# Optimization experiments

Measured on AMD Instinct MI355X. Metric: run time of the kernel, lower is better.

Reference implementation:

```python
import jax, jax.numpy as jnp
import numpy as np

B, T, C, H, NUM_EDGE_TYPES = 2, 512, 256, 8, 16


def setup_inputs() -> dict:
    key = jax.random.key(0)
    ks = jax.random.split(key, 8)
    init = 0.02
    x = jax.random.normal(ks[0], (B, T, C), dtype=jnp.float32)
    bias_matrix = jax.random.randint(ks[1], (B, T, T), 0, NUM_EDGE_TYPES)
    w_attn = jax.random.normal(ks[2], (C, 3 * C), dtype=jnp.float32) * init
    w_proj = jax.random.normal(ks[3], (C, C), dtype=jnp.float32) * init
    w_edge_k = jax.random.normal(ks[4], (C, C), dtype=jnp.float32) * init
    w_edge_v = jax.random.normal(ks[5], (C, C), dtype=jnp.float32) * init
    edge_emb_table = jax.random.normal(ks[6], (NUM_EDGE_TYPES, C), dtype=jnp.float32)
    attn_bias_table = jax.random.normal(ks[7], (NUM_EDGE_TYPES, H), dtype=jnp.float32)
    return {
        "x": x,
        "bias_matrix": bias_matrix,
        "w_attn": w_attn,
        "w_proj": w_proj,
        "w_edge_k": w_edge_k,
        "w_edge_v": w_edge_v,
        "edge_emb_table": edge_emb_table,
        "attn_bias_table": attn_bias_table,
    }


def reference(x, bias_matrix, w_attn, w_proj, w_edge_k, w_edge_v,
              edge_emb_table, attn_bias_table):
    b, t, c = x.shape
    h = attn_bias_table.shape[1]
    e = c // h
    scale = jnp.sqrt(jnp.asarray(e, x.dtype))

    qkv = x @ w_attn                              # (B,T,3C)
    q, k, v = jnp.split(qkv, 3, axis=-1)
    # (B,H,T,E)
    q = q.reshape(b, t, h, e).transpose(0, 2, 1, 3)
    k = k.reshape(b, t, h, e).transpose(0, 2, 1, 3)
    v = v.reshape(b, t, h, e).transpose(0, 2, 1, 3)

    # edge-type embeddings and per-pair k/v modulation, (B,T,T,H,E)
    ee = edge_emb_table[bias_matrix]              # (B,T,T,C)
    e_k = (ee @ w_edge_k).reshape(b, t, t, h, e)
    e_v = (ee @ w_edge_v).reshape(b, t, t, h, e)

    # scores[b,h,i,j] = sum_e q[b,h,i,e] * k[b,h,j,e] * e_k[b, j, i, h, e]
    # (torch: e_k permuted to (B,H,j,i,E), broadcast-multiplied by k then
    #  contracted with q via 'bhie,bhjie->bhij')
    scores = jnp.einsum('bhie,bhje,bjihe->bhij', q, k, e_k) / scale

    causal = jnp.tril(jnp.ones((t, t), dtype=bool))  # (T,T)
    scores = jnp.where(causal, scores, -jnp.inf)

    # edge-type attention bias: (B,T,T,H) -> (B,H,T,T), zeroed above diagonal
    bias = attn_bias_table[bias_matrix].transpose(0, 3, 1, 2)
    bias = jnp.where(causal, bias, jnp.zeros((), bias.dtype))

    attn = jax.nn.softmax(scores + bias, axis=-1)  # (B,H,T,T)

    # y[b,h,i,e] = sum_j attn[b,h,i,j] * v[b,h,j,e] * e_v[b, j, i, h, e]
    y = jnp.einsum('bhij,bhje,bjihe->bhie', attn, v, e_v)
    y = y.transpose(0, 2, 1, 3).reshape(b, t, c)
    return y @ w_proj
```

## Files before the change

kernel.cpp:

```cpp
#include <hip/hip_runtime.h>
#include <hip/hip_bf16.h>
#include <math.h>

#define Bdim 2
#define Tdim 512
#define Cdim 256
#define Hdim 8
#define Edim 32
#define NTYPES 16
#define TI 8
#define JT 128

__global__ __launch_bounds__(256) void pre_kernel(
    const float* __restrict__ A, const float* __restrict__ Bw,
    const float* __restrict__ emb, const float* __restrict__ wk,
    const float* __restrict__ wv,
    float* __restrict__ qT, float* __restrict__ kT, float* __restrict__ vT,
    float* __restrict__ ekt, float* __restrict__ evt)
{
    __shared__ float smem[16 * 34 + 16 * 64];
    int tid = threadIdx.x;

    if (blockIdx.x >= 384) {
        int t = blockIdx.x - 384;
        float* se = smem;
        se[tid] = emb[t * Cdim + tid];
        __syncthreads();
        float a = 0.f, b = 0.f;
        for (int k = 0; k < Cdim; ++k) {
            float ev = se[k];
            a = fmaf(ev, wk[k * Cdim + tid], a);
            b = fmaf(ev, wv[k * Cdim + tid], b);
        }
        ekt[t * Cdim + tid] = a;
        evt[t * Cdim + tid] = b;
        return;
    }

    const int N = 3 * Cdim;
    const int K = Cdim;
    float (*As)[34] = (float(*)[34])smem;
    float (*Bs)[64] = (float(*)[64])(smem + 16 * 34);
    int m0 = (blockIdx.x / 12) * 32;
    int n0 = (blockIdx.x % 12) * 64;
    int tr = tid >> 4, tc = tid & 15;
    float acc[2][4] = {};
    int bkr = tid >> 4, bcq = (tid & 15) * 4;

    for (int k0 = 0; k0 < K; k0 += 16) {
        if (tid < 128) {
            int r = tid >> 2, kq = (tid & 3) * 4;
            float4 av = *(const float4*)(A + (size_t)(m0 + r) * K + k0 + kq);
            As[kq + 0][r] = av.x;
            As[kq + 1][r] = av.y;
            As[kq + 2][r] = av.z;
            As[kq + 3][r] = av.w;
        }
        float4 bv = *(const float4*)(Bw + (size_t)(k0 + bkr) * N + n0 + bcq);
        *(float4*)&Bs[bkr][bcq] = bv;
        __syncthreads();
#pragma unroll
        for (int kk = 0; kk < 16; ++kk) {
            float2 a2 = *(float2*)&As[kk][tr * 2];
            float4 b4 = *(float4*)&Bs[kk][tc * 4];
            acc[0][0] = fmaf(a2.x, b4.x, acc[0][0]);
            acc[0][1] = fmaf(a2.x, b4.y, acc[0][1]);
            acc[0][2] = fmaf(a2.x, b4.z, acc[0][2]);
            acc[0][3] = fmaf(a2.x, b4.w, acc[0][3]);
            acc[1][0] = fmaf(a2.y, b4.x, acc[1][0]);
            acc[1][1] = fmaf(a2.y, b4.y, acc[1][1]);
            acc[1][2] = fmaf(a2.y, b4.z, acc[1][2]);
            acc[1][3] = fmaf(a2.y, b4.w, acc[1][3]);
        }
        __syncthreads();
    }
    int sec = n0 >> 8;
    float* dst = (sec == 0) ? qT : (sec == 1) ? kT : vT;
    int cc0 = (n0 & 255) + tc * 4;
    int h = cc0 >> 5;
    int e0 = cc0 & 31;
#pragma unroll
    for (int i = 0; i < 2; ++i) {
        int m = m0 + tr * 2 + i;
        int bq = m >> 9, t = m & (Tdim - 1);
        float4 val = make_float4(acc[i][0], acc[i][1], acc[i][2], acc[i][3]);
        *(float4*)&dst[(((size_t)bq * Hdim + h) * Tdim + t) * Edim + e0] = val;
    }
}

__global__ __launch_bounds__(512, 4) void attn_kernel(
    const float* __restrict__ qT, const float* __restrict__ kT,
    const float* __restrict__ vT, const int* __restrict__ bm,
    const float* __restrict__ ekt, const float* __restrict__ evt,
    const float* __restrict__ abt, float* __restrict__ y)
{
    __shared__ float kv[JT][36];
    __shared__ float qm[TI][NTYPES][36];
    __shared__ float ss[TI][516];
    __shared__ unsigned int st1pf[Tdim];
    __shared__ unsigned int st2pf[Tdim];
    __shared__ float sekt[NTYPES][36];
    __shared__ float sevt[NTYPES][36];
    __shared__ float sq[TI][36];
    __shared__ float sabt[NTYPES];
    __shared__ float sinv[TI];

    float* spart = (float*)qm;

    const int pairIdx = blockIdx.x;
    const int bh = blockIdx.y;
    const int h = bh & (Hdim - 1);
    const int b = bh >> 3;
    const int tid = threadIdx.x;
    const int wave = tid >> 6;
    const int lane = tid & 63;
    const float inv_scale = 0.17677669529663687f;

    const float* qbase = qT + (size_t)bh * Tdim * Edim;
    const float* kbase = kT + (size_t)bh * Tdim * Edim;
    const float* vbase = vT + (size_t)bh * Tdim * Edim;
    const int* bmb = bm + (size_t)b * Tdim * Tdim;

    if (tid < 128) {
        int t = tid >> 3, eq = tid & 7;
        *(float4*)&sekt[t][eq * 4] = *(const float4*)&ekt[t * Cdim + h * Edim + eq * 4];
        *(float4*)&sevt[t][eq * 4] = *(const float4*)&evt[t * Cdim + h * Edim + eq * 4];
    }
    if (tid < NTYPES) sabt[tid] = abt[tid * Hdim + h];

    for (int rep = 0; rep < 2; ++rep) {
        int tau = rep ? (63 - pairIdx) : pairIdx;
        int i0 = tau * TI;
        int imax = i0 + TI - 1;
        int njt = (imax >> 7) + 1;
        int jmax = njt << 7;

        __syncthreads();

        if (tid < TI * 8) {
            int r = tid >> 3, eq = tid & 7;
            *(float4*)&sq[r][eq * 4] =
                *(const float4*)&qbase[(size_t)(i0 + r) * Edim + eq * 4];
        }
        if (tid < jmax) {
            const int* rowp = bmb + (size_t)tid * Tdim + i0;
            int4 lo = *(const int4*)rowp;
            int4 hi = *(const int4*)(rowp + 4);
            st1pf[tid] =
                ((unsigned)(lo.x & 15)) | (((unsigned)(lo.y & 15)) << 4) |
                (((unsigned)(lo.z & 15)) << 8) | (((unsigned)(lo.w & 15)) << 12) |
                (((unsigned)(hi.x & 15)) << 16) | (((unsigned)(hi.y & 15)) << 20) |
                (((unsigned)(hi.z & 15)) << 24) | (((unsigned)(hi.w & 15)) << 28);
            unsigned w2 = 0;
#pragma unroll
            for (int iiq = 0; iiq < 8; ++iiq)
                w2 |= ((unsigned)(bmb[(size_t)(i0 + iiq) * Tdim + tid] & 15)) << (iiq * 4);
            st2pf[tid] = w2;
        }
        {
            int r0 = tid >> 3, eq0 = tid & 7;
            *(float4*)&kv[r0][eq0 * 4] =
                *(const float4*)&kbase[(size_t)r0 * Edim + eq0 * 4];
            int idx1 = tid + 512;
            int r1 = idx1 >> 3, eq1 = idx1 & 7;
            *(float4*)&kv[r1][eq1 * 4] =
                *(const float4*)&kbase[(size_t)r1 * Edim + eq1 * 4];
        }
        __syncthreads();
        for (int idx = tid; idx < TI * NTYPES * 8; idx += 512) {
            int eq = idx & 7;
            int t = (idx >> 3) & (NTYPES - 1);
            int r = idx >> 7;
            float4 qv = *(float4*)&sq[r][eq * 4];
            float4 ev = *(float4*)&sekt[t][eq * 4];
            float4 o;
            o.x = qv.x * ev.x; o.y = qv.y * ev.y;
            o.z = qv.z * ev.z; o.w = qv.w * ev.w;
            *(float4*)&qm[r][t][eq * 4] = o;
        }

        for (int jt = 0; jt < njt; ++jt) {
            int j0 = jt << 7;
            if (jt > 0) {
                __syncthreads();
                for (int idx = tid; idx < JT * 8; idx += 512) {
                    int r = idx >> 3, eq = idx & 7;
                    *(float4*)&kv[r][eq * 4] =
                        *(const float4*)&kbase[(size_t)(j0 + r) * Edim + eq * 4];
                }
            }
            __syncthreads();

            int jsub = wave & 1;
            int jl = (jsub << 6) + lane;
            int j = j0 + jl;
            float4 k4[8];
#pragma unroll
            for (int eq = 0; eq < 8; ++eq) k4[eq] = *(float4*)&kv[jl][eq * 4];
            unsigned tp = st1pf[j];
            unsigned tp2 = st2pf[j];

#pragma unroll
            for (int u = 0; u < 2; ++u) {
                int ii = (wave >> 1) + (u << 2);
                int i = i0 + ii;
                if (j0 + (jsub << 6) > i) continue;
                int t1 = (tp >> (ii * 4)) & 15;
                int t2 = (tp2 >> (ii * 4)) & 15;
                float s = 0.f;
#pragma unroll
                for (int eq = 0; eq < 8; ++eq) {
                    float4 qv = *(float4*)&qm[ii][t1][eq * 4];
                    s = fmaf(qv.x, k4[eq].x, s);
                    s = fmaf(qv.y, k4[eq].y, s);
                    s = fmaf(qv.z, k4[eq].z, s);
                    s = fmaf(qv.w, k4[eq].w, s);
                }
                if (j <= i) ss[ii][j] = s * inv_scale + sabt[t2];
            }
        }
        __syncthreads();

        {
            int r0 = tid >> 3, eq0 = tid & 7;
            *(float4*)&kv[r0][eq0 * 4] =
                *(const float4*)&vbase[(size_t)r0 * Edim + eq0 * 4];
            int idx1 = tid + 512;
            int r1 = idx1 >> 3, eq1 = idx1 & 7;
            *(float4*)&kv[r1][eq1 * 4] =
                *(const float4*)&vbase[(size_t)r1 * Edim + eq1 * 4];
        }
        {
            int ii = wave;
            int i = i0 + ii;
            float m = -1e30f;
            for (int j = lane; j <= i; j += 64) m = fmaxf(m, ss[ii][j]);
            for (int off = 32; off; off >>= 1) m = fmaxf(m, __shfl_xor(m, off));
            float sum = 0.f;
            for (int j = lane; j <= i; j += 64) {
                float p = __expf(ss[ii][j] - m);
                ss[ii][j] = p;
                sum += p;
            }
            for (int off = 32; off; off >>= 1) sum += __shfl_xor(sum, off);
            if (lane == 0) sinv[ii] = 1.0f / sum;
        }

        float4 acc[TI];
#pragma unroll
        for (int ii = 0; ii < TI; ++ii) acc[ii] = make_float4(0.f, 0.f, 0.f, 0.f);
        int gid = tid >> 3;
        int eqg = tid & 7;
        for (int jt = 0; jt < njt; ++jt) {
            int j0 = jt << 7;
            if (jt > 0) {
                __syncthreads();
                for (int idx = tid; idx < JT * 8; idx += 512) {
                    int r = idx >> 3, eq = idx & 7;
                    *(float4*)&kv[r][eq * 4] =
                        *(const float4*)&vbase[(size_t)(j0 + r) * Edim + eq * 4];
                }
            }
            __syncthreads();
#pragma unroll
            for (int sub = 0; sub < 2; ++sub) {
                int jl = (sub << 6) + gid;
                int j = j0 + jl;
                float4 v4 = *(float4*)&kv[jl][eqg * 4];
                unsigned tp = st1pf[j];
#pragma unroll
                for (int ii = 0; ii < TI; ++ii) {
                    int i = i0 + ii;
                    if (j0 + (sub << 6) > i) continue;
                    float p = (j <= i) ? ss[ii][j] : 0.f;
                    int t1 = (tp >> (ii * 4)) & 15;
                    float4 ev = *(float4*)&sevt[t1][eqg * 4];
                    acc[ii].x = fmaf(p * ev.x, v4.x, acc[ii].x);
                    acc[ii].y = fmaf(p * ev.y, v4.y, acc[ii].y);
                    acc[ii].z = fmaf(p * ev.z, v4.z, acc[ii].z);
                    acc[ii].w = fmaf(p * ev.w, v4.w, acc[ii].w);
                }
            }
        }
#pragma unroll
        for (int ii = 0; ii < TI; ++ii) {
#pragma unroll
            for (int m = 8; m <= 32; m <<= 1) {
                acc[ii].x += __shfl_xor(acc[ii].x, m);
                acc[ii].y += __shfl_xor(acc[ii].y, m);
                acc[ii].z += __shfl_xor(acc[ii].z, m);
                acc[ii].w += __shfl_xor(acc[ii].w, m);
            }
        }
        if (lane < 8) {
#pragma unroll
            for (int ii = 0; ii < TI; ++ii)
                *(float4*)&spart[((wave * TI + ii) << 5) + lane * 4] = acc[ii];
        }
        __syncthreads();
        if (tid < TI * Edim) {
            int ii = tid >> 5, e = tid & 31;
            float yv = 0.f;
#pragma unroll
            for (int w = 0; w < 8; ++w) yv += spart[((w * TI + ii) << 5) + e];
            yv *= sinv[ii];
            y[((size_t)(b * Tdim + i0 + ii)) * Cdim + h * Edim + e] = yv;
        }
    }
}

__global__ __launch_bounds__(256) void proj_gemm_kernel(
    const float* __restrict__ A, const float* __restrict__ Bw,
    float* __restrict__ out)
{
    const int N = Cdim;
    const int K = Cdim;
    __shared__ float As[16][34];
    __shared__ float Bs[16][64];
    int m0 = blockIdx.y * 32;
    int n0 = blockIdx.x * 64;
    int tid = threadIdx.x;
    int tr = tid >> 4, tc = tid & 15;
    float acc[2][4] = {};
    int bkr = tid >> 4, bcq = (tid & 15) * 4;

    for (int k0 = 0; k0 < K; k0 += 16) {
        if (tid < 128) {
            int r = tid >> 2, kq = (tid & 3) * 4;
            float4 av = *(const float4*)(A + (size_t)(m0 + r) * K + k0 + kq);
            As[kq + 0][r] = av.x;
            As[kq + 1][r] = av.y;
            As[kq + 2][r] = av.z;
            As[kq + 3][r] = av.w;
        }
        float4 bv = *(const float4*)(Bw + (size_t)(k0 + bkr) * N + n0 + bcq);
        *(float4*)&Bs[bkr][bcq] = bv;
        __syncthreads();
#pragma unroll
        for (int kk = 0; kk < 16; ++kk) {
            float2 a2 = *(float2*)&As[kk][tr * 2];
            float4 b4 = *(float4*)&Bs[kk][tc * 4];
            acc[0][0] = fmaf(a2.x, b4.x, acc[0][0]);
            acc[0][1] = fmaf(a2.x, b4.y, acc[0][1]);
            acc[0][2] = fmaf(a2.x, b4.z, acc[0][2]);
            acc[0][3] = fmaf(a2.x, b4.w, acc[0][3]);
            acc[1][0] = fmaf(a2.y, b4.x, acc[1][0]);
            acc[1][1] = fmaf(a2.y, b4.y, acc[1][1]);
            acc[1][2] = fmaf(a2.y, b4.z, acc[1][2]);
            acc[1][3] = fmaf(a2.y, b4.w, acc[1][3]);
        }
        __syncthreads();
    }
#pragma unroll
    for (int i = 0; i < 2; ++i) {
        int m = m0 + tr * 2 + i;
        float4 val = make_float4(acc[i][0], acc[i][1], acc[i][2], acc[i][3]);
        *(float4*)&out[(size_t)m * N + n0 + tc * 4] = val;
    }
}

extern "C" void kernel_launch(void* const* d_in, const int* in_sizes, int n_in,
                              void* d_out, int out_size, void* d_ws, size_t ws_size,
                              hipStream_t stream) {
    (void)in_sizes; (void)n_in; (void)out_size; (void)ws_size;
    const float* x = (const float*)d_in[0];
    const int* bias_matrix = (const int*)d_in[1];
    const float* w_attn = (const float*)d_in[2];
    const float* w_proj = (const float*)d_in[3];
    const float* w_edge_k = (const float*)d_in[4];
    const float* w_edge_v = (const float*)d_in[5];
    const float* edge_emb = (const float*)d_in[6];
    const float* attn_bias = (const float*)d_in[7];
    float* out = (float*)d_out;

    const size_t n_qkv = (size_t)Bdim * Hdim * Tdim * Edim;
    float* ws = (float*)d_ws;
    float* qT = ws;
    float* kT = qT + n_qkv;
    float* vT = kT + n_qkv;
    float* y = vT + n_qkv;
    float* ekt = y + (size_t)Bdim * Tdim * Cdim;
    float* evt = ekt + (size_t)NTYPES * Cdim;

    pre_kernel<<<400, 256, 0, stream>>>(x, w_attn, edge_emb, w_edge_k, w_edge_v,
                                        qT, kT, vT, ekt, evt);
    attn_kernel<<<dim3(32, 16), 512, 0, stream>>>(qT, kT, vT, bias_matrix,
                                                  ekt, evt, attn_bias, y);
    proj_gemm_kernel<<<dim3(4, 32), 256, 0, stream>>>(y, w_proj, out);
}
```

Baseline: 133.5 us.

## Double-buffer K/V tiles with register prefetch and XOR-swizzled shared layout

Converts the single K/V shared-memory tile into a ping-pong pair. The next 128-row tile is loaded into registers before the current tile's score or accumulation work and stored into the other buffer afterwards, so global-load latency overlaps compute and one barrier per tile is dropped. The padded row stride of 36 is replaced by a 32-float stride with an XOR swizzle to avoid bank conflicts. This costs extra shared memory and registers for the prefetch, which at 512 threads with a launch bound of 4 could reduce occupancy.

```diff
diff --git a/kernel.cpp b/kernel.cpp
--- a/kernel.cpp
+++ b/kernel.cpp
@@ -94,7 +94,7 @@
     const float* __restrict__ ekt, const float* __restrict__ evt,
     const float* __restrict__ abt, float* __restrict__ y)
 {
-    __shared__ float kv[JT][36];
+    __shared__ float kv[2][JT][32];
     __shared__ float qm[TI][NTYPES][36];
     __shared__ float ss[TI][516];
     __shared__ unsigned int st1pf[Tdim];
@@ -120,6 +120,10 @@
     const float* kbase = kT + (size_t)bh * Tdim * Edim;
     const float* vbase = vT + (size_t)bh * Tdim * Edim;
     const int* bmb = bm + (size_t)b * Tdim * Tdim;
+
+    const int sr0 = tid >> 3;
+    const int seq4 = (tid & 7) << 2;
+    const int ssw = seq4 ^ ((sr0 & 7) << 2);
 
     if (tid < 128) {
         int t = tid >> 3, eq = tid & 7;
@@ -157,15 +161,10 @@
                 w2 |= ((unsigned)(bmb[(size_t)(i0 + iiq) * Tdim + tid] & 15)) << (iiq * 4);
             st2pf[tid] = w2;
         }
-        {
-            int r0 = tid >> 3, eq0 = tid & 7;
-            *(float4*)&kv[r0][eq0 * 4] =
-                *(const float4*)&kbase[(size_t)r0 * Edim + eq0 * 4];
-            int idx1 = tid + 512;
-            int r1 = idx1 >> 3, eq1 = idx1 & 7;
-            *(float4*)&kv[r1][eq1 * 4] =
-                *(const float4*)&kbase[(size_t)r1 * Edim + eq1 * 4];
-        }
+        *(float4*)&kv[0][sr0][ssw] =
+            *(const float4*)&kbase[((size_t)sr0 << 5) + seq4];
+        *(float4*)&kv[0][sr0 + 64][ssw] =
+            *(const float4*)&kbase[(((size_t)sr0 + 64) << 5) + seq4];
         __syncthreads();
         for (int idx = tid; idx < TI * NTYPES * 8; idx += 512) {
             int eq = idx & 7;
@@ -178,25 +177,27 @@
             o.z = qv.z * ev.z; o.w = qv.w * ev.w;
             *(float4*)&qm[r][t][eq * 4] = o;
         }
-
+        __syncthreads();
+
+        int cur = 0;
         for (int jt = 0; jt < njt; ++jt) {
             int j0 = jt << 7;
-            if (jt > 0) {
-                __syncthreads();
-                for (int idx = tid; idx < JT * 8; idx += 512) {
-                    int r = idx >> 3, eq = idx & 7;
-                    *(float4*)&kv[r][eq * 4] =
-                        *(const float4*)&kbase[(size_t)(j0 + r) * Edim + eq * 4];
-                }
-            }
-            __syncthreads();
+            const bool pf = (jt + 1) < njt;
+            float4 n0, n1;
+            if (pf) {
+                const float* src = kbase + ((size_t)(j0 + 128) << 5);
+                n0 = *(const float4*)(src + ((size_t)sr0 << 5) + seq4);
+                n1 = *(const float4*)(src + (((size_t)sr0 + 64) << 5) + seq4);
+            }
 
             int jsub = wave & 1;
             int jl = (jsub << 6) + lane;
             int j = j0 + jl;
+            const int xsw = (jl & 7) << 2;
             float4 k4[8];
 #pragma unroll
-            for (int eq = 0; eq < 8; ++eq) k4[eq] = *(float4*)&kv[jl][eq * 4];
+            for (int eq = 0; eq < 8; ++eq)
+                k4[eq] = *(float4*)&kv[cur][jl][(eq << 2) ^ xsw];
             unsigned tp = st1pf[j];
             unsigned tp2 = st2pf[j];
 
@@ -218,18 +219,20 @@
                 }
                 if (j <= i) ss[ii][j] = s * inv_scale + sabt[t2];
             }
-        }
-        __syncthreads();
-
-        {
-            int r0 = tid >> 3, eq0 = tid & 7;
-            *(float4*)&kv[r0][eq0 * 4] =
-                *(const float4*)&vbase[(size_t)r0 * Edim + eq0 * 4];
-            int idx1 = tid + 512;
-            int r1 = idx1 >> 3, eq1 = idx1 & 7;
-            *(float4*)&kv[r1][eq1 * 4] =
-                *(const float4*)&vbase[(size_t)r1 * Edim + eq1 * 4];
-        }
+
+            if (pf) {
+                *(float4*)&kv[cur ^ 1][sr0][ssw] = n0;
+                *(float4*)&kv[cur ^ 1][sr0 + 64][ssw] = n1;
+            }
+            __syncthreads();
+            cur ^= 1;
+        }
+
+        *(float4*)&kv[0][sr0][ssw] =
+            *(const float4*)&vbase[((size_t)sr0 << 5) + seq4];
+        *(float4*)&kv[0][sr0 + 64][ssw] =
+            *(const float4*)&vbase[(((size_t)sr0 + 64) << 5) + seq4];
+
         {
             int ii = wave;
             int i = i0 + ii;
@@ -245,28 +248,28 @@
             for (int off = 32; off; off >>= 1) sum += __shfl_xor(sum, off);
             if (lane == 0) sinv[ii] = 1.0f / sum;
         }
+        __syncthreads();
 
         float4 acc[TI];
 #pragma unroll
         for (int ii = 0; ii < TI; ++ii) acc[ii] = make_float4(0.f, 0.f, 0.f, 0.f);
         int gid = tid >> 3;
-        int eqg = tid & 7;
+        int eqg4 = (tid & 7) << 2;
+        cur = 0;
         for (int jt = 0; jt < njt; ++jt) {
             int j0 = jt << 7;
-            if (jt > 0) {
-                __syncthreads();
-                for (int idx = tid; idx < JT * 8; idx += 512) {
-                    int r = idx >> 3, eq = idx & 7;
-                    *(float4*)&kv[r][eq * 4] =
-                        *(const float4*)&vbase[(size_t)(j0 + r) * Edim + eq * 4];
-                }
-            }
-            __syncthreads();
+            const bool pf = (jt + 1) < njt;
+            float4 n0, n1;
+            if (pf) {
+                const float* src = vbase + ((size_t)(j0 + 128) << 5);
+                n0 = *(const float4*)(src + ((size_t)sr0 << 5) + seq4);
+                n1 = *(const float4*)(src + (((size_t)sr0 + 64) << 5) + seq4);
+            }
 #pragma unroll
             for (int sub = 0; sub < 2; ++sub) {
                 int jl = (sub << 6) + gid;
                 int j = j0 + jl;
-                float4 v4 = *(float4*)&kv[jl][eqg * 4];
+                float4 v4 = *(float4*)&kv[cur][jl][eqg4 ^ ((jl & 7) << 2)];
                 unsigned tp = st1pf[j];
 #pragma unroll
                 for (int ii = 0; ii < TI; ++ii) {
@@ -274,13 +277,19 @@
                     if (j0 + (sub << 6) > i) continue;
                     float p = (j <= i) ? ss[ii][j] : 0.f;
                     int t1 = (tp >> (ii * 4)) & 15;
-                    float4 ev = *(float4*)&sevt[t1][eqg * 4];
+                    float4 ev = *(float4*)&sevt[t1][eqg4];
                     acc[ii].x = fmaf(p * ev.x, v4.x, acc[ii].x);
                     acc[ii].y = fmaf(p * ev.y, v4.y, acc[ii].y);
                     acc[ii].z = fmaf(p * ev.z, v4.z, acc[ii].z);
                     acc[ii].w = fmaf(p * ev.w, v4.w, acc[ii].w);
                 }
             }
+            if (pf) {
+                *(float4*)&kv[cur ^ 1][sr0][ssw] = n0;
+                *(float4*)&kv[cur ^ 1][sr0 + 64][ssw] = n1;
+            }
+            __syncthreads();
+            cur ^= 1;
         }
 #pragma unroll
         for (int ii = 0; ii < TI; ++ii) {
```

Result: no change. 135.3 us (+1.3%).
